# Kernel tuning notes

Measured on AMD Instinct MI355X. Metric: run time of the kernel, lower is better.

The kernel has to match this reference:

```python
import jax, jax.numpy as jnp
import numpy as np

B, L = 8, 2048
H_IN = 20
K1, K2 = 16, 32
NG = 32            # n_gaussians
D1, D2 = 7, 5      # gaussian kernel input dims
DM = 128           # outer product out_features
DH = 32            # attribute embedding out_features
IDX_MAX = 8.0      # index_distance_max


def _gather(x, idx):
    # x: (B,L,H), idx: (B,L,K) -> (B,L,K,H)
    b = jnp.arange(x.shape[0])[:, None, None]
    return x[b, idx]


def _neighbors(frames, kmax):
    c = frames[:, :, 0, :]                      # centers (B,L,3)
    sq = jnp.sum(c * c, axis=-1)
    d2 = sq[:, :, None] + sq[:, None, :] - 2.0 * jnp.einsum('bld,bmd->blm', c, c)
    _, idx = jax.lax.top_k(-d2, kmax)           # self (d2=0) lands in slot 0
    return idx


def _coords(frames, seq_idx, idx):
    c = frames[:, :, 0, :]
    axes = frames[:, :, 1:4, :]                 # local frame axes of center node
    z = frames[:, :, 3, :]
    c_j = _gather(c, idx)
    z_j = _gather(z, idx)
    delta = c_j - c[:, :, None, :]              # (B,L,K,3)
    dist = jnp.sqrt(jnp.sum(delta * delta, -1, keepdims=True) + 1e-12)
    eucl = jnp.einsum('blkd,blad->blka', delta, axes)   # neighbor coords in local frame
    zdotz = jnp.sum(z[:, :, None, :] * z_j, -1, keepdims=True)
    deltadotz = jnp.sum(delta * z_j, -1, keepdims=True) / dist
    zdotdelta = jnp.sum(z[:, :, None, :] * delta, -1, keepdims=True) / dist
    sidx = seq_idx.astype(jnp.float32)          # (B,L,1)
    idist = jnp.clip(jnp.abs(_gather(sidx, idx) - sidx[:, :, None, :]), 0.0, IDX_MAX)
    return eucl, dist, zdotz, deltadotz, zdotdelta, idist


def _gaussian(x, centers, prec):
    # full-covariance Gaussian kernel: exp(-0.5 ||P_n (x - mu_n)||^2)
    diff = x[..., None] - centers               # (...,d,NG)
    y = jnp.einsum('...dn,dkn->...kn', diff, prec)
    return jnp.exp(-0.5 * jnp.sum(y * y, axis=-2))


def _forward(aa_attributes, aa_frame, aa_indices,
             gk1_centers, gk1_prec, op_kernel, op_bias,
             emb_W, emb_b, beta_W, beta_b, selfatt_W, selfatt_b,
             crossatt_W, crossatt_b, nodef_W, nodef_b,
             gk2_centers, gk2_prec, emb2_W, emb2_b):
    # --- neighborhood 1: euclidian + index_distance + ZdotZ + (DeltadotZ,ZdotDelta)
    idx1 = _neighbors(aa_frame, K1)
    eucl, _, zz, dz, zd, idist = _coords(aa_frame, aa_indices, idx1)
    coords1 = jnp.concatenate([eucl, idist, zz, dz, zd], axis=-1)   # (B,L,K1,7)
    neigh_attr = _gather(aa_attributes, idx1)                        # (B,L,K1,20)
    g1 = _gaussian(coords1, gk1_centers, gk1_prec)                   # (B,L,K1,NG)
    # outer-product embedding: sum over neighbors and (gaussian x attribute) pairs
    filt = jnp.einsum('blkg,blkh,gho->blo', g1, neigh_attr, op_kernel) + op_bias
    f = jax.nn.relu(filt)                                            # (B,L,128)
    emb = jax.nn.relu(f @ emb_W + emb_b)                             # (B,L,32)
    beta = jax.nn.relu(emb @ beta_W + beta_b)                        # (B,L,1)
    satt = jax.nn.relu(emb @ selfatt_W + selfatt_b)                  # (B,L,1)
    catt = jax.nn.relu(emb @ crossatt_W + crossatt_b)                # (B,L,1)
    nodef = jax.nn.relu(emb @ nodef_W + nodef_b)                     # (B,L,2)
    # --- neighborhood 2: distance + ZdotZ + (DeltadotZ,ZdotDelta) + index_distance
    idx2 = _neighbors(aa_frame, K2)
    _, dist2, zz2, dz2, zd2, idist2 = _coords(aa_frame, aa_indices, idx2)
    coords2 = jnp.concatenate([dist2, zz2, dz2, zd2, idist2], axis=-1)  # (B,L,K2,5)
    att_local = _gather(catt, idx2)                                  # (B,L,K2,1)
    nodef_local = _gather(nodef, idx2)                               # (B,L,K2,2)
    g2 = _gaussian(coords2, gk2_centers, gk2_prec)                   # (B,L,K2,NG)
    gw = jax.nn.relu(g2 @ emb2_W + emb2_b)                           # (B,L,K2,1)
    # --- graph attention aggregation (self slot is k=0)
    e = att_local.at[:, :, 0, :].set(satt)
    logits = beta[:, :, None, :] * e
    logits = logits - jnp.max(logits, axis=2, keepdims=True)
    w = gw * jnp.exp(logits)
    a = w / (jnp.sum(w, axis=2, keepdims=True) + 1e-6)               # (B,L,K2,1)
    out = jnp.sum(a * nodef_local, axis=2)                           # (B,L,2)
    return out


def setup_inputs():
    key = jax.random.key(0)
    ks = jax.random.split(key, 16)
    eye1 = jnp.tile(jnp.eye(D1, dtype=jnp.float32)[:, :, None], (1, 1, NG))
    eye2 = jnp.tile(jnp.eye(D2, dtype=jnp.float32)[:, :, None], (1, 1, NG))
    return {
        'aa_attributes': jax.random.normal(ks[0], (B, L, H_IN), jnp.float32),
        'aa_frame': jax.random.normal(ks[1], (B, L, 4, 3), jnp.float32),
        'aa_indices': jnp.arange(B * L, dtype=jnp.int32).reshape(B, L, 1),
        'gk1_centers': 0.1 * jax.random.normal(ks[2], (D1, NG), jnp.float32),
        'gk1_prec': eye1 + 0.05 * jax.random.normal(ks[3], (D1, D1, NG), jnp.float32),
        'op_kernel': 0.05 * jax.random.normal(ks[4], (NG, H_IN, DM), jnp.float32),
        'op_bias': jnp.zeros((DM,), jnp.float32),
        'emb_W': jax.random.normal(ks[5], (DM, DH), jnp.float32) / np.sqrt(DM),
        'emb_b': jnp.zeros((DH,), jnp.float32),
        'beta_W': jax.random.normal(ks[6], (DH, 1), jnp.float32) / np.sqrt(DH),
        'beta_b': jnp.zeros((1,), jnp.float32),
        'selfatt_W': jax.random.normal(ks[7], (DH, 1), jnp.float32) / np.sqrt(DH),
        'selfatt_b': jnp.zeros((1,), jnp.float32),
        'crossatt_W': jax.random.normal(ks[8], (DH, 1), jnp.float32) / np.sqrt(DH),
        'crossatt_b': jnp.zeros((1,), jnp.float32),
        'nodef_W': jax.random.normal(ks[9], (DH, 2), jnp.float32) / np.sqrt(DH),
        'nodef_b': jnp.zeros((2,), jnp.float32),
        'gk2_centers': 0.1 * jax.random.normal(ks[10], (D2, NG), jnp.float32),
        'gk2_prec': eye2 + 0.05 * jax.random.normal(ks[11], (D2, D2, NG), jnp.float32),
        'emb2_W': jax.random.normal(ks[12], (NG, 1), jnp.float32) / np.sqrt(NG),
        'emb2_b': jnp.zeros((1,), jnp.float32),
    }


def reference(aa_attributes, aa_frame, aa_indices,
              gk1_centers, gk1_prec, op_kernel, op_bias,
              emb_W, emb_b, beta_W, beta_b, selfatt_W, selfatt_b,
              crossatt_W, crossatt_b, nodef_W, nodef_b,
              gk2_centers, gk2_prec, emb2_W, emb2_b):
    return _forward(aa_attributes, aa_frame, aa_indices,
                    gk1_centers, gk1_prec, op_kernel, op_bias,
                    emb_W, emb_b, beta_W, beta_b, selfatt_W, selfatt_b,
                    crossatt_W, crossatt_b, nodef_W, nodef_b,
                    gk2_centers, gk2_prec, emb2_W, emb2_b)
```

## Files before the change

kernel.cpp:

```cpp
#include <hip/hip_runtime.h>

typedef unsigned int u32;
typedef unsigned long long u64;
typedef unsigned short u16;

#define NL 2048

typedef __attribute__((ext_vector_type(8))) short bf16x8;
typedef __attribute__((ext_vector_type(16))) float f32x16;

__device__ __forceinline__ u16 to_bf16(float f) {
  u32 b = __float_as_uint(f);
  b += 0x7FFFu + ((b >> 16) & 1u);
  return (u16)(b >> 16);
}

__device__ __forceinline__ void gload_lds16(const void* g, void* l) {
  __builtin_amdgcn_global_load_lds(
      (const __attribute__((address_space(1))) u32*)g,
      (__attribute__((address_space(3))) u32*)l, 16, 0, 0);
}

__device__ __forceinline__ u32 sort64_u32(u32 v, int lane) {
#pragma unroll
  for (int k = 2; k <= 64; k <<= 1) {
#pragma unroll
    for (int j = k >> 1; j > 0; j >>= 1) {
      u32 p = (u32)__shfl_xor((int)v, j, 64);
      bool lower = ((lane & j) == 0);
      bool asc = ((lane & k) == 0);
      u32 lo = v < p ? v : p;
      u32 hi = v < p ? p : v;
      v = (lower == asc) ? lo : hi;
    }
  }
  return v;
}

__global__ __launch_bounds__(512) void knn_prep_kernel(
    const float* __restrict__ frames, int* __restrict__ idx32,
    const float* __restrict__ opW, const float* __restrict__ embW,
    const float* __restrict__ betaW, const float* __restrict__ sattW,
    const float* __restrict__ cattW, const float* __restrict__ nodW,
    const float* __restrict__ betaB, const float* __restrict__ sattB,
    const float* __restrict__ cattB, const float* __restrict__ nodB,
    u16* __restrict__ opWt, u16* __restrict__ embWt, float* __restrict__ w5,
    float* __restrict__ b5) {
  __shared__ union U {
    struct {
      float4 cand[2048];
      u64 comp[8][256];
    } k;
    float tp[128 * 73];
  } sm;
  const int bx = blockIdx.x;
  const int tid = threadIdx.x;

  if (bx >= 2048) {
    if (bx < 2058) {
      const int k0 = (bx - 2048) * 64;
#pragma unroll
      for (int j = 0; j < 4; j++) {
        int f = tid + j * 512;
        int kk = f >> 5;
        int o4 = (f & 31) * 4;
        float4 v = *(const float4*)(opW + (size_t)(k0 + kk) * 128 + o4);
        sm.tp[(o4 + 0) * 73 + kk] = v.x;
        sm.tp[(o4 + 1) * 73 + kk] = v.y;
        sm.tp[(o4 + 2) * 73 + kk] = v.z;
        sm.tp[(o4 + 3) * 73 + kk] = v.w;
      }
      __syncthreads();
      u32* ow = (u32*)opWt;
#pragma unroll
      for (int j = 0; j < 8; j++) {
        int f = tid + j * 512;
        int o = f >> 5, q = f & 31;
        float lo = sm.tp[o * 73 + q * 2];
        float hi = sm.tp[o * 73 + q * 2 + 1];
        ow[o * 320 + (k0 >> 1) + q] = (u32)to_bf16(lo) | ((u32)to_bf16(hi) << 16);
      }
    } else {
      for (int f = tid; f < 4096; f += 512) {
        int j = f >> 7, kk = f & 127;
        embWt[f] = to_bf16(embW[(size_t)kk * 32 + j]);
      }
      if (tid < 160) {
        int h = tid >> 5, j = tid & 31;
        float v = (h == 0) ? betaW[j]
                  : (h == 1) ? sattW[j]
                  : (h == 2) ? cattW[j]
                  : (h == 3) ? nodW[j * 2]
                             : nodW[j * 2 + 1];
        w5[j * 8 + h] = v;
      } else if (tid < 165) {
        int h = tid - 160;
        float v = (h == 0) ? betaB[0]
                  : (h == 1) ? sattB[0]
                  : (h == 2) ? cattB[0]
                  : (h == 3) ? nodB[0]
                             : nodB[1];
        b5[h] = v;
      }
    }
    return;
  }

  const int w = tid >> 6, lane = tid & 63;
  const int query = bx * 8 + w;
  const int b = query >> 11, lq = query & (NL - 1);

#pragma unroll
  for (int i = 0; i < 4; i++) {
    int l = tid + i * 512;
    const float* fp = frames + (size_t)(b * NL + l) * 12;
    float4 fr = *(const float4*)fp;
    sm.k.cand[l] = make_float4(fr.x, fr.y, fr.z,
                               fr.x * fr.x + fr.y * fr.y + fr.z * fr.z);
  }
  __syncthreads();

  float4 me = sm.k.cand[lq];
  u32 k[32];
  u32 m = 0xFFFFFFFFu;
#pragma unroll
  for (int i = 0; i < 32; i++) {
    float4 c = sm.k.cand[i * 64 + lane];
    float dot = c.x * me.x + c.y * me.y + c.z * me.z;
    float d2 = (me.w + c.w) - 2.0f * dot;
    u32 kb = __float_as_uint(d2);
    u32 key = kb ^ ((u32)((int)kb >> 31) | 0x80000000u);
    k[i] = key;
    m = key < m ? key : m;
  }

  u32 ms = sort64_u32(m, lane);
  u32 T0 = (u32)__shfl((int)ms, 31, 64);

  int base = 0;
#pragma unroll
  for (int i = 0; i < 32; i++) {
    bool flag = (k[i] <= T0);
    u64 mask = __ballot(flag);
    if (flag) {
      u32 rank = __builtin_amdgcn_mbcnt_hi(
          (u32)(mask >> 32), __builtin_amdgcn_mbcnt_lo((u32)mask, 0u));
      int pos = base + (int)rank;
      if (pos < 256) sm.k.comp[w][pos] = ((u64)k[i] << 32) | (u32)(i * 64 + lane);
    }
    base += (int)__popcll(mask);
  }
  int cnt = base < 256 ? base : 256;
  __syncthreads();

  if (cnt <= 64) {
    int pz = cnt + lane;
    if (pz < 64) sm.k.comp[w][pz] = ~0ull;
    u64 e0 = sm.k.comp[w][lane];
    int r0 = 0;
#pragma unroll
    for (int mi = 0; mi < 64; mi++) {
      u64 em = sm.k.comp[w][mi];
      r0 += (em < e0) ? 1 : 0;
    }
    if (r0 < 32) idx32[(size_t)query * 32 + r0] = (int)(e0 & 0xFFFFFFFFull);
  } else {
    for (int b0 = 0; b0 < cnt; b0 += 64) {
      bool live = (b0 + lane < cnt);
      u64 e = live ? sm.k.comp[w][b0 + lane] : ~0ull;
      int r = 0;
      for (int mi = 0; mi < cnt; mi++) {
        u64 em = sm.k.comp[w][mi];
        r += (em < e) ? 1 : 0;
      }
      if (live && r < 32)
        idx32[(size_t)query * 32 + r] = (int)(e & 0xFFFFFFFFull);
    }
  }
}

__global__ __launch_bounds__(256) void stage1_kernel(
    const float* __restrict__ frames, const float* __restrict__ attrs,
    const int* __restrict__ aaidx, const float* __restrict__ cen1,
    const float* __restrict__ prec1, const int* __restrict__ idx32,
    u16* __restrict__ outer) {
  __shared__ float sCoord[4 * 16 * 8];
  __shared__ float sAttrT[4 * 20 * 16];
  __shared__ float sG1T[4 * 32 * 17];
  const int tid = threadIdx.x;
  const int pt = tid >> 6, lane = tid & 63;
  const int pid = blockIdx.x * 4 + pt;
  const int b = pid >> 11;
  const int g = lane & 31;

  float pr[7][7], cn[7];
#pragma unroll
  for (int d = 0; d < 7; d++) {
    cn[d] = cen1[d * 32 + g];
#pragma unroll
    for (int kk = 0; kk < 7; kk++) pr[d][kk] = prec1[(d * 7 + kk) * 32 + g];
  }

  if (lane < 16) {
    int n = lane;
    int j = idx32[pid * 32 + n];
    int jg = b * NL + j;
    const float* fs = frames + (size_t)pid * 12;
    const float* fj = frames + (size_t)jg * 12;
    float4 A0 = *(const float4*)(fs);
    float4 A1 = *(const float4*)(fs + 4);
    float4 A2 = *(const float4*)(fs + 8);
    float4 B0 = *(const float4*)(fj);
    float4 B2 = *(const float4*)(fj + 8);
    float dx = B0.x - A0.x, dy = B0.y - A0.y, dzc = B0.z - A0.z;
    float a0x = A0.w, a0y = A1.x, a0z = A1.y;
    float a1x = A1.z, a1y = A1.w, a1z = A2.x;
    float a2x = A2.y, a2y = A2.z, a2z = A2.w;
    float zjx = B2.y, zjy = B2.z, zjz = B2.w;
    float dd = dx * dx + dy * dy + dzc * dzc + 1e-12f;
    float dist = sqrtf(dd);
    float e0 = dx * a0x + dy * a0y + dzc * a0z;
    float e1 = dx * a1x + dy * a1y + dzc * a1z;
    float e2 = dx * a2x + dy * a2y + dzc * a2z;
    float zz = a2x * zjx + a2y * zjy + a2z * zjz;
    float dzv = (dx * zjx + dy * zjy + dzc * zjz) / dist;
    float zdv = (a2x * dx + a2y * dy + a2z * dzc) / dist;
    float si = (float)aaidx[pid];
    float sj = (float)aaidx[jg];
    float idist = fminf(fabsf(sj - si), 8.0f);
    float* cr = sCoord + pt * 128 + n * 8;
    cr[0] = e0; cr[1] = e1; cr[2] = e2; cr[3] = idist;
    cr[4] = zz; cr[5] = dzv; cr[6] = zdv;
    const float* ar = attrs + (size_t)jg * 20;
    float4 q0 = *(const float4*)(ar);
    float4 q1 = *(const float4*)(ar + 4);
    float4 q2 = *(const float4*)(ar + 8);
    float4 q3 = *(const float4*)(ar + 12);
    float4 q4 = *(const float4*)(ar + 16);
    float av[20] = {q0.x, q0.y, q0.z, q0.w, q1.x, q1.y, q1.z, q1.w,
                    q2.x, q2.y, q2.z, q2.w, q3.x, q3.y, q3.z, q3.w,
                    q4.x, q4.y, q4.z, q4.w};
#pragma unroll
    for (int h = 0; h < 20; h++) sAttrT[pt * 320 + h * 16 + n] = av[h];
  }
  __syncthreads();
  {
    const int nh = lane >> 5;
#pragma unroll
    for (int i = 0; i < 8; i++) {
      int n = nh * 8 + i;
      const float* cr = sCoord + pt * 128 + n * 8;
      float df[7];
#pragma unroll
      for (int d = 0; d < 7; d++) df[d] = cr[d] - cn[d];
      float s = 0.0f;
#pragma unroll
      for (int kk = 0; kk < 7; kk++) {
        float y = 0.0f;
#pragma unroll
        for (int d = 0; d < 7; d++) y = fmaf(df[d], pr[d][kk], y);
        s = fmaf(y, y, s);
      }
      sG1T[pt * 544 + g * 17 + n] = __expf(-0.5f * s);
    }
  }
  __syncthreads();
  {
    const int hg = lane >> 5;
    float g16[16];
#pragma unroll
    for (int n = 0; n < 16; n++) g16[n] = sG1T[pt * 544 + g * 17 + n];
    u32* orow = (u32*)(outer + (size_t)pid * 640) + (g * 20 + hg * 10) / 2;
#pragma unroll
    for (int i = 0; i < 5; i++) {
      int h0 = hg * 10 + i * 2, h1 = h0 + 1;
      float a0 = 0.f, a1 = 0.f;
#pragma unroll
      for (int c = 0; c < 4; c++) {
        float4 v0 = *(float4*)&sAttrT[pt * 320 + h0 * 16 + c * 4];
        float4 v1 = *(float4*)&sAttrT[pt * 320 + h1 * 16 + c * 4];
        a0 = fmaf(v0.x, g16[c * 4 + 0], a0);
        a0 = fmaf(v0.y, g16[c * 4 + 1], a0);
        a0 = fmaf(v0.z, g16[c * 4 + 2], a0);
        a0 = fmaf(v0.w, g16[c * 4 + 3], a0);
        a1 = fmaf(v1.x, g16[c * 4 + 0], a1);
        a1 = fmaf(v1.y, g16[c * 4 + 1], a1);
        a1 = fmaf(v1.z, g16[c * 4 + 2], a1);
        a1 = fmaf(v1.w, g16[c * 4 + 3], a1);
      }
      orow[i] = (u32)to_bf16(a0) | ((u32)to_bf16(a1) << 16);
    }
  }
}

__global__ __launch_bounds__(256) void gemm_kernel(
    const u16* __restrict__ outer,
    const u16* __restrict__ opWt,
    const float* __restrict__ opB,
    const u16* __restrict__ embWt,
    const float* __restrict__ embB,
    const float* __restrict__ w5,
    const float* __restrict__ b5,
    float* __restrict__ head8) {
  __shared__ char smem[40960];
  const int tid = threadIdx.x;
  const int w = tid >> 6, lane = tid & 63;
  const int p0 = blockIdx.x * 32;
  const int lr = lane >> 3, lc = lane & 7;
  const int gsw = lc ^ lr;
  const int m = lane & 31, kh = lane >> 5;

  f32x16 acc;
#pragma unroll
  for (int r = 0; r < 16; r++) acc[r] = 0.f;

  const u16* gA = outer + (size_t)(p0 + w * 8 + lr) * 640 + gsw * 8;
#pragma unroll
  for (int cc = 0; cc < 10; cc++)
    gload_lds16(gA + cc * 64, smem + cc * 4096 + w * 1024);
  __syncthreads();

  const u16* gB = opWt + (size_t)(w * 32 + m) * 640;
#pragma unroll
  for (int cc = 0; cc < 10; cc++) {
#pragma unroll
    for (int s = 0; s < 4; s++) {
      int pg = (s * 2 + kh) ^ (m & 7);
      bf16x8 av = *(bf16x8*)(smem + cc * 4096 + m * 128 + pg * 16);
      bf16x8 bv = *(const bf16x8*)(gB + cc * 64 + s * 16 + kh * 8);
      acc = __builtin_amdgcn_mfma_f32_32x32x16_bf16(av, bv, acc, 0, 0, 0);
    }
  }
  __syncthreads();

  const int o = w * 32 + m;
  float bo = opB[o];
#pragma unroll
  for (int i = 0; i < 2; i++) {
    int j = w * 8 + i * 4 + (lane >> 4);
    int ge = (lane & 15) ^ (j & 7);
    gload_lds16(embWt + j * 128 + ge * 8, smem + 8192 + w * 2048 + i * 1024);
  }
  u16* sFb = (u16*)smem;
#pragma unroll
  for (int r = 0; r < 16; r++) {
    int mm = (r & 3) + 8 * (r >> 2) + 4 * kh;
    float v = fmaxf(acc[r] + bo, 0.f);
    int pg = (o >> 3) ^ (mm & 7);
    sFb[mm * 128 + pg * 8 + (o & 7)] = to_bf16(v);
  }
  __syncthreads();

  f32x16 acc2;
#pragma unroll
  for (int r = 0; r < 16; r++) acc2[r] = 0.f;
#pragma unroll
  for (int t2 = 0; t2 < 2; t2++) {
    int gg = (w * 2 + t2) * 2 + kh;
    int pg = gg ^ (m & 7);
    bf16x8 av = *(bf16x8*)(smem + m * 256 + pg * 16);
    bf16x8 bv = *(bf16x8*)(smem + 8192 + m * 256 + pg * 16);
    acc2 = __builtin_amdgcn_mfma_f32_32x32x16_bf16(av, bv, acc2, 0, 0, 0);
  }
  float* scr = (float*)(smem + 16384) + w * 1024;
#pragma unroll
  for (int r = 0; r < 16; r++) {
    int mm = (r & 3) + 8 * (r >> 2) + 4 * kh;
    scr[mm * 32 + m] = acc2[r];
  }
  __syncthreads();

  {
    float* sc = (float*)(smem + 16384);
    int i4 = tid * 4;
    float4 v0 = *(float4*)(sc + i4);
    float4 v1 = *(float4*)(sc + 1024 + i4);
    float4 v2 = *(float4*)(sc + 2048 + i4);
    float4 v3 = *(float4*)(sc + 3072 + i4);
    int pp = tid >> 3, j0 = (tid & 7) * 4;
    float4 eb = *(const float4*)(embB + j0);
    float4 e;
    e.x = fmaxf(v0.x + v1.x + v2.x + v3.x + eb.x, 0.f);
    e.y = fmaxf(v0.y + v1.y + v2.y + v3.y + eb.y, 0.f);
    e.z = fmaxf(v0.z + v1.z + v2.z + v3.z + eb.z, 0.f);
    e.w = fmaxf(v0.w + v1.w + v2.w + v3.w + eb.w, 0.f);
    *(float4*)((float*)smem + pp * 36 + j0) = e;
  }
  __syncthreads();

  if (tid < 160) {
    int h = tid >> 5, p = tid & 31;
    const float* sE = (const float*)smem + p * 36;
    float a = b5[h];
#pragma unroll
    for (int j = 0; j < 32; j++) a = fmaf(sE[j], w5[j * 8 + h], a);
    a = fmaxf(a, 0.f);
    int slot = (h < 2) ? (h + 4) : (h - 2);
    head8[(size_t)(p0 + p) * 8 + slot] = a;
  }
}

__global__ __launch_bounds__(256) void stage2_kernel(
    const float* __restrict__ frames, const int* __restrict__ aaidx,
    const float* __restrict__ cen2, const float* __restrict__ prec2,
    const float* __restrict__ emb2W, const float* __restrict__ emb2B,
    const int* __restrict__ idx32, const float* __restrict__ head8,
    float* __restrict__ out) {
  __shared__ float sCoord[4 * 32 * 5];
  __shared__ float sG2[4 * 32 * 33];
  const int tid = threadIdx.x;
  const int pt = tid >> 6, lane = tid & 63;
  const int pid = blockIdx.x * 4 + pt;
  const int b = pid >> 11;
  const int g = lane & 31;

  float pr[5][5], cn[5];
#pragma unroll
  for (int d = 0; d < 5; d++) {
    cn[d] = cen2[d * 32 + g];
#pragma unroll
    for (int kk = 0; kk < 5; kk++) pr[d][kk] = prec2[(d * 5 + kk) * 32 + g];
  }

  float4 hv = make_float4(0.f, 0.f, 0.f, 0.f);
  float betaS = 0.f, sattS = 0.f;
  if (lane < 32) {
    int n = lane;
    int j = idx32[pid * 32 + n];
    int jg = b * NL + j;
    const float* fs = frames + (size_t)pid * 12;
    const float* fj = frames + (size_t)jg * 12;
    float4 A0 = *(const float4*)(fs);
    float4 A2 = *(const float4*)(fs + 8);
    float4 B0 = *(const float4*)(fj);
    float4 B2 = *(const float4*)(fj + 8);
    float dx = B0.x - A0.x, dy = B0.y - A0.y, dzc = B0.z - A0.z;
    float a2x = A2.y, a2y = A2.z, a2z = A2.w;
    float zjx = B2.y, zjy = B2.z, zjz = B2.w;
    float dd = dx * dx + dy * dy + dzc * dzc + 1e-12f;
    float dist = sqrtf(dd);
    float zz = a2x * zjx + a2y * zjy + a2z * zjz;
    float dzv = (dx * zjx + dy * zjy + dzc * zjz) / dist;
    float zdv = (a2x * dx + a2y * dy + a2z * dzc) / dist;
    float si = (float)aaidx[pid];
    float sj = (float)aaidx[jg];
    float idist = fminf(fabsf(sj - si), 8.0f);
    float* cr = sCoord + pt * 160 + n * 5;
    cr[0] = dist; cr[1] = zz; cr[2] = dzv; cr[3] = zdv; cr[4] = idist;
    hv = *(const float4*)(head8 + (size_t)jg * 8);
    betaS = head8[(size_t)pid * 8 + 4];
    sattS = head8[(size_t)pid * 8 + 5];
  }
  __syncthreads();
  {
    const int nh = lane >> 5;
#pragma unroll
    for (int i = 0; i < 16; i++) {
      int n = nh * 16 + i;
      const float* cr = sCoord + pt * 160 + n * 5;
      float df[5];
#pragma unroll
      for (int d = 0; d < 5; d++) df[d] = cr[d] - cn[d];
      float s = 0.0f;
#pragma unroll
      for (int kk = 0; kk < 5; kk++) {
        float y = 0.0f;
#pragma unroll
        for (int d = 0; d < 5; d++) y = fmaf(df[d], pr[d][kk], y);
        s = fmaf(y, y, s);
      }
      sG2[pt * 1056 + n * 33 + g] = __expf(-0.5f * s);
    }
  }
  __syncthreads();
  if (lane < 32) {
    int n = lane;
    float gw = emb2B[0];
#pragma unroll 8
    for (int gg = 0; gg < 32; gg++)
      gw = fmaf(sG2[pt * 1056 + n * 33 + gg], emb2W[gg], gw);
    gw = fmaxf(gw, 0.0f);
    float e = (n == 0) ? sattS : hv.x;
    float logit = betaS * e;
    float mx = logit;
#pragma unroll
    for (int d = 1; d < 32; d <<= 1) mx = fmaxf(mx, __shfl_xor(mx, d, 64));
    float wv = gw * __expf(logit - mx);
    float S = wv;
#pragma unroll
    for (int d = 1; d < 32; d <<= 1) S += __shfl_xor(S, d, 64);
    float a = wv / (S + 1e-6f);
    float o0 = a * hv.y, o1 = a * hv.z;
#pragma unroll
    for (int d = 1; d < 32; d <<= 1) {
      o0 += __shfl_xor(o0, d, 64);
      o1 += __shfl_xor(o1, d, 64);
    }
    if (n == 0) {
      out[pid * 2 + 0] = o0;
      out[pid * 2 + 1] = o1;
    }
  }
}

extern "C" void kernel_launch(void* const* d_in, const int* in_sizes, int n_in,
                              void* d_out, int out_size, void* d_ws, size_t ws_size,
                              hipStream_t stream) {
  const float* attrs = (const float*)d_in[0];
  const float* frames = (const float*)d_in[1];
  const int* aaidx = (const int*)d_in[2];
  const float* cen1 = (const float*)d_in[3];
  const float* prec1 = (const float*)d_in[4];
  const float* opW = (const float*)d_in[5];
  const float* opB = (const float*)d_in[6];
  const float* embW = (const float*)d_in[7];
  const float* embB = (const float*)d_in[8];
  const float* betaW = (const float*)d_in[9];
  const float* betaB = (const float*)d_in[10];
  const float* sattW = (const float*)d_in[11];
  const float* sattB = (const float*)d_in[12];
  const float* cattW = (const float*)d_in[13];
  const float* cattB = (const float*)d_in[14];
  const float* nodW = (const float*)d_in[15];
  const float* nodB = (const float*)d_in[16];
  const float* cen2 = (const float*)d_in[17];
  const float* prec2 = (const float*)d_in[18];
  const float* emb2W = (const float*)d_in[19];
  const float* emb2B = (const float*)d_in[20];
  float* out = (float*)d_out;

  char* ws = (char*)d_ws;
  int* idx32 = (int*)ws;
  u16* outer_bf = (u16*)(ws + 2097152);
  float* head8 = (float*)(ws + 23068672);
  u16* opWt = (u16*)(ws + 23592960);
  u16* embWt = (u16*)(ws + 23756800);
  float* w5 = (float*)(ws + 23764992);
  float* b5 = (float*)(ws + 23766016);

  knn_prep_kernel<<<dim3(2059), dim3(512), 0, stream>>>(
      frames, idx32, opW, embW, betaW, sattW, cattW, nodW, betaB, sattB,
      cattB, nodB, opWt, embWt, w5, b5);
  stage1_kernel<<<dim3(4096), dim3(256), 0, stream>>>(frames, attrs, aaidx, cen1,
                                                      prec1, idx32, outer_bf);
  gemm_kernel<<<dim3(512), dim3(256), 0, stream>>>(outer_bf, opWt, opB, embWt,
                                                   embB, w5, b5, head8);
  stage2_kernel<<<dim3(4096), dim3(256), 0, stream>>>(frames, aaidx, cen2, prec2,
                                                      emb2W, emb2B, idx32, head8, out);
}
```

Before: 184.0 us.

## Bitonic-sort kNN candidates, spread attr gather, pack stage2 at 32 lanes per point

In the common kNN path (64 or fewer candidates), the O(64^2) rank-counting loop over shared memory is replaced by a 64-lane bitonic sort over 64-bit keys built from shuffles. In stage1, the neighbor attribute gather moves from 16 lanes each loading 80 bytes to all 64 lanes each loading one float4. Stage2 now maps each point to 32 threads instead of 64, so 8 points fit per block and the grid is halved, which removes idle half-wavefronts. The cost is more shuffle traffic in the sort and a longer per-thread loop in stage2.

```diff
diff --git a/kernel.cpp b/kernel.cpp
--- a/kernel.cpp
+++ b/kernel.cpp
@@ -19,6 +19,12 @@
   __builtin_amdgcn_global_load_lds(
       (const __attribute__((address_space(1))) u32*)g,
       (__attribute__((address_space(3))) u32*)l, 16, 0, 0);
+}
+
+__device__ __forceinline__ u64 shfl_xor64(u64 v, int m) {
+  int lo = __shfl_xor((int)(u32)v, m, 64);
+  int hi = __shfl_xor((int)(u32)(v >> 32), m, 64);
+  return ((u64)(u32)hi << 32) | (u32)lo;
 }
 
 __device__ __forceinline__ u32 sort64_u32(u32 v, int lane) {
@@ -31,6 +37,22 @@
       bool asc = ((lane & k) == 0);
       u32 lo = v < p ? v : p;
       u32 hi = v < p ? p : v;
+      v = (lower == asc) ? lo : hi;
+    }
+  }
+  return v;
+}
+
+__device__ __forceinline__ u64 sort64_u64(u64 v, int lane) {
+#pragma unroll
+  for (int k = 2; k <= 64; k <<= 1) {
+#pragma unroll
+    for (int j = k >> 1; j > 0; j >>= 1) {
+      u64 p = shfl_xor64(v, j);
+      bool lower = ((lane & j) == 0);
+      bool asc = ((lane & k) == 0);
+      u64 lo = v < p ? v : p;
+      u64 hi = v < p ? p : v;
       v = (lower == asc) ? lo : hi;
     }
   }
@@ -157,13 +179,9 @@
     int pz = cnt + lane;
     if (pz < 64) sm.k.comp[w][pz] = ~0ull;
     u64 e0 = sm.k.comp[w][lane];
-    int r0 = 0;
-#pragma unroll
-    for (int mi = 0; mi < 64; mi++) {
-      u64 em = sm.k.comp[w][mi];
-      r0 += (em < e0) ? 1 : 0;
-    }
-    if (r0 < 32) idx32[(size_t)query * 32 + r0] = (int)(e0 & 0xFFFFFFFFull);
+    u64 s = sort64_u64(e0, lane);
+    if (lane < 32)
+      idx32[(size_t)query * 32 + lane] = (int)(s & 0xFFFFFFFFull);
   } else {
     for (int b0 = 0; b0 < cnt; b0 += 64) {
       bool live = (b0 + lane < cnt);
@@ -199,6 +217,26 @@
     cn[d] = cen1[d * 32 + g];
 #pragma unroll
     for (int kk = 0; kk < 7; kk++) pr[d][kk] = prec1[(d * 7 + kk) * 32 + g];
+  }
+
+  {
+    const int nn = lane >> 2, q = lane & 3;
+    int j2 = idx32[pid * 32 + nn];
+    int jg2 = b * NL + j2;
+    const float* ar = attrs + (size_t)jg2 * 20;
+    float4 v = *(const float4*)(ar + q * 4);
+    float* aw = sAttrT + pt * 320 + nn;
+    aw[(q * 4 + 0) * 16] = v.x;
+    aw[(q * 4 + 1) * 16] = v.y;
+    aw[(q * 4 + 2) * 16] = v.z;
+    aw[(q * 4 + 3) * 16] = v.w;
+    if (q == 3) {
+      float4 v4 = *(const float4*)(ar + 16);
+      aw[16 * 16] = v4.x;
+      aw[17 * 16] = v4.y;
+      aw[18 * 16] = v4.z;
+      aw[19 * 16] = v4.w;
+    }
   }
 
   if (lane < 16) {
@@ -231,17 +269,6 @@
     float* cr = sCoord + pt * 128 + n * 8;
     cr[0] = e0; cr[1] = e1; cr[2] = e2; cr[3] = idist;
     cr[4] = zz; cr[5] = dzv; cr[6] = zdv;
-    const float* ar = attrs + (size_t)jg * 20;
-    float4 q0 = *(const float4*)(ar);
-    float4 q1 = *(const float4*)(ar + 4);
-    float4 q2 = *(const float4*)(ar + 8);
-    float4 q3 = *(const float4*)(ar + 12);
-    float4 q4 = *(const float4*)(ar + 16);
-    float av[20] = {q0.x, q0.y, q0.z, q0.w, q1.x, q1.y, q1.z, q1.w,
-                    q2.x, q2.y, q2.z, q2.w, q3.x, q3.y, q3.z, q3.w,
-                    q4.x, q4.y, q4.z, q4.w};
-#pragma unroll
-    for (int h = 0; h < 20; h++) sAttrT[pt * 320 + h * 16 + n] = av[h];
   }
   __syncthreads();
   {
@@ -406,13 +433,13 @@
     const float* __restrict__ emb2W, const float* __restrict__ emb2B,
     const int* __restrict__ idx32, const float* __restrict__ head8,
     float* __restrict__ out) {
-  __shared__ float sCoord[4 * 32 * 5];
-  __shared__ float sG2[4 * 32 * 33];
+  __shared__ float sCoord[8 * 32 * 5];
+  __shared__ float sG2[8 * 32 * 33];
   const int tid = threadIdx.x;
-  const int pt = tid >> 6, lane = tid & 63;
-  const int pid = blockIdx.x * 4 + pt;
+  const int pt = tid >> 5, n = tid & 31;
+  const int pid = blockIdx.x * 8 + pt;
   const int b = pid >> 11;
-  const int g = lane & 31;
+  const int g = n;
 
   float pr[5][5], cn[5];
 #pragma unroll
@@ -422,10 +449,9 @@
     for (int kk = 0; kk < 5; kk++) pr[d][kk] = prec2[(d * 5 + kk) * 32 + g];
   }
 
-  float4 hv = make_float4(0.f, 0.f, 0.f, 0.f);
-  float betaS = 0.f, sattS = 0.f;
-  if (lane < 32) {
-    int n = lane;
+  float4 hv;
+  float betaS, sattS;
+  {
     int j = idx32[pid * 32 + n];
     int jg = b * NL + j;
     const float* fs = frames + (size_t)pid * 12;
@@ -453,11 +479,9 @@
   }
   __syncthreads();
   {
-    const int nh = lane >> 5;
-#pragma unroll
-    for (int i = 0; i < 16; i++) {
-      int n = nh * 16 + i;
-      const float* cr = sCoord + pt * 160 + n * 5;
+#pragma unroll 8
+    for (int i = 0; i < 32; i++) {
+      const float* cr = sCoord + pt * 160 + i * 5;
       float df[5];
 #pragma unroll
       for (int d = 0; d < 5; d++) df[d] = cr[d] - cn[d];
@@ -469,12 +493,11 @@
         for (int d = 0; d < 5; d++) y = fmaf(df[d], pr[d][kk], y);
         s = fmaf(y, y, s);
       }
-      sG2[pt * 1056 + n * 33 + g] = __expf(-0.5f * s);
-    }
-  }
-  __syncthreads();
-  if (lane < 32) {
-    int n = lane;
+      sG2[pt * 1056 + i * 33 + g] = __expf(-0.5f * s);
+    }
+  }
+  __syncthreads();
+  {
     float gw = emb2B[0];
 #pragma unroll 8
     for (int gg = 0; gg < 32; gg++)
@@ -545,6 +568,6 @@
                                                       prec1, idx32, outer_bf);
   gemm_kernel<<<dim3(512), dim3(256), 0, stream>>>(outer_bf, opWt, opB, embWt,
                                                    embB, w5, b5, head8);
-  stage2_kernel<<<dim3(4096), dim3(256), 0, stream>>>(frames, aaidx, cen2, prec2,
+  stage2_kernel<<<dim3(2048), dim3(256), 0, stream>>>(frames, aaidx, cen2, prec2,
                                                       emb2W, emb2B, idx32, head8, out);
 }
```

Measured after the change: 185.7 us. No clear change (+0.9%).
